# Kernel optimization log

Measured on AMD Instinct MI355X. Metric: run time of the kernel, lower is better.

The kernel has to match this reference:

```python
import jax, jax.numpy as jnp
import numpy as np

N, B, C, H = 2048, 2, 1024, 16
HD = C // H


def setup_inputs() -> dict:
    key = jax.random.key(0)
    ks = jax.random.split(key, 11)
    s = 0.02
    return {
        "query": jax.random.normal(ks[0], (N, B, C), jnp.float32),
        "key": jax.random.normal(ks[1], (N, B, C), jnp.float32),
        "value": jax.random.normal(ks[2], (B, N, C), jnp.float32),
        "num_heads": H,
        "Wq": jax.random.normal(ks[3], (C, C), jnp.float32) * s,
        "bq": jnp.zeros((C,), jnp.float32),
        "Wk": jax.random.normal(ks[4], (C, HD), jnp.float32) * s,
        "bk": jnp.zeros((HD,), jnp.float32),
        "Wv": jax.random.normal(ks[5], (C, HD), jnp.float32) * s,
        "bv": jnp.zeros((HD,), jnp.float32),
        "Wp": jax.random.normal(ks[6], (C, C), jnp.float32) * s,
        "bp": jnp.zeros((C,), jnp.float32),
    }


def reference(query, key, value, num_heads, Wq, bq, Wk, bk, Wv, bv, Wp, bp):
    # query/key arrive seq-first (N,B,C); permute to batch-first as in torch code
    k_in = jnp.transpose(key, (1, 0, 2))    # (B, Nk, C)
    q_in = jnp.transpose(query, (1, 0, 2))  # (B, Nq, C)
    Bsz, Nq, Cd = q_in.shape
    hd = Cd // num_heads
    scale = hd ** -0.5

    # shared single K/V head (MQA)
    k = k_in @ Wk + bk                      # (B, Nk, hd)
    v = value @ Wv + bv                     # (B, Nk, hd)
    q = (q_in @ Wq + bq).reshape(Bsz, Nq, num_heads, hd)
    q = jnp.transpose(q, (0, 2, 1, 3)) * scale  # (B, H, Nq, hd)

    attn = jnp.einsum('bhqd,bkd->bhqk', q, k)   # (B, H, Nq, Nk)
    attn = jax.nn.softmax(attn, axis=-1)
    x = jnp.einsum('bhqk,bkd->bhqd', attn, v)   # (B, H, Nq, hd)
    x = jnp.transpose(x, (0, 2, 1, 3)).reshape(Bsz, Nq, Cd)
    x = x @ Wp + bp
    return jnp.transpose(x, (1, 0, 2))          # (Nq, B, C)
```

## Files before the change

kernel.cpp:

```cpp
#include <hip/hip_runtime.h>
#include <hip/hip_bf16.h>

#define DI __device__ __forceinline__

typedef float f32x4 __attribute__((ext_vector_type(4)));
typedef float f32x16 __attribute__((ext_vector_type(16)));
typedef short s16x8 __attribute__((ext_vector_type(8)));
typedef unsigned short u16x4 __attribute__((ext_vector_type(4)));
typedef unsigned long long u64;


DI unsigned short f2bf(float x) {
  union { float f; unsigned u; } v; v.f = x;
  unsigned r = 0x7fffu + ((v.u >> 16) & 1u);
  return (unsigned short)((v.u + r) >> 16);
}

DI unsigned cvtpk(float lo, float hi) {
  unsigned u;
  asm("v_cvt_pk_bf16_f32 %0, %1, %2" : "=v"(u) : "v"(lo), "v"(hi));
  return u;
}

DI f32x16 zero16() {
  f32x16 z;
#pragma unroll
  for (int i = 0; i < 16; ++i) z[i] = 0.f;
  return z;
}

DI float max16(const f32x16& a) {
  float m0 = fmaxf(a[0], a[1]),  m1 = fmaxf(a[2], a[3]);
  float m2 = fmaxf(a[4], a[5]),  m3 = fmaxf(a[6], a[7]);
  float m4 = fmaxf(a[8], a[9]),  m5 = fmaxf(a[10], a[11]);
  float m6 = fmaxf(a[12], a[13]), m7 = fmaxf(a[14], a[15]);
  m0 = fmaxf(m0, m1); m2 = fmaxf(m2, m3); m4 = fmaxf(m4, m5); m6 = fmaxf(m6, m7);
  return fmaxf(fmaxf(m0, m2), fmaxf(m4, m6));
}

DI float sum16(const f32x16& a) {
  float s0 = a[0] + a[1],  s1 = a[2] + a[3];
  float s2 = a[4] + a[5],  s3 = a[6] + a[7];
  float s4 = a[8] + a[9],  s5 = a[10] + a[11];
  float s6 = a[12] + a[13], s7 = a[14] + a[15];
  s0 += s1; s2 += s3; s4 += s5; s6 += s7;
  return (s0 + s2) + (s4 + s6);
}

DI void gll16(const void* g, void* l) {
  __builtin_amdgcn_global_load_lds(
      (const __attribute__((address_space(1))) void*)g,
      (__attribute__((address_space(3))) void*)l, 16, 0, 0);
}

DI f32x16 mfma32(s16x8 a, s16x8 b, f32x16 c) {
  return __builtin_amdgcn_mfma_f32_32x32x16_bf16(a, b, c, 0, 0, 0);
}

DI f32x4 mfma16(s16x8 a, s16x8 b, f32x4 c) {
  return __builtin_amdgcn_mfma_f32_16x16x32_bf16(a, b, c, 0, 0, 0);
}

__global__ __launch_bounds__(256) void wconv_kernel(
    const float* __restrict__ Wq, const float* __restrict__ Wk,
    const float* __restrict__ Wv, const float* __restrict__ Wp,
    unsigned short* __restrict__ WqT, unsigned short* __restrict__ WkT,
    unsigned short* __restrict__ WvT, unsigned short* __restrict__ WpT)
{
  int bid = blockIdx.x;
  const float* W; unsigned short* WT; int Ncols; int base;
  if (bid < 512)       { W = Wq; WT = WqT; Ncols = 1024; base = bid; }
  else if (bid < 1024) { W = Wp; WT = WpT; Ncols = 1024; base = bid - 512; }
  else if (bid < 1056) { W = Wk; WT = WkT; Ncols = 64;   base = bid - 1024; }
  else                 { W = Wv; WT = WvT; Ncols = 64;   base = bid - 1056; }
  int nb = base >> 5, kb = base & 31;
  int n = nb * 64 + (threadIdx.x & 63);
  int k = kb * 32 + (threadIdx.x >> 6) * 8;
  float f[8];
#pragma unroll
  for (int i = 0; i < 8; ++i) f[i] = W[(size_t)(k + i) * Ncols + n];
  union { unsigned u[4]; s16x8 v; } x;
#pragma unroll
  for (int i = 0; i < 4; ++i) x.u[i] = cvtpk(f[2 * i], f[2 * i + 1]);
  *(s16x8*)(WT + (size_t)n * 1024 + k) = x.v;
}

__global__ __launch_bounds__(256) void cvt1_kernel(
    const float* __restrict__ q, unsigned short* __restrict__ qbf)
{
  int gid = blockIdx.x * 256 + threadIdx.x;
  int row = gid >> 7;
  int c8 = (gid & 127) << 3;
  int b = row >> 11, n = row & 2047;
  size_t soff = ((size_t)n * 2 + b) * 1024 + c8;
  f32x4 v0 = *(const f32x4*)(q + soff);
  f32x4 v1 = *(const f32x4*)(q + soff + 4);
  union { unsigned u[4]; s16x8 v; } x;
  x.u[0] = cvtpk(v0.x, v0.y); x.u[1] = cvtpk(v0.z, v0.w);
  x.u[2] = cvtpk(v1.x, v1.y); x.u[3] = cvtpk(v1.z, v1.w);
  *(s16x8*)(qbf + (size_t)row * 1024 + c8) = x.v;
}

template<int MODE>
__global__ __launch_bounds__(256) void gemm16_kernel(
    const unsigned short* __restrict__ A, const unsigned short* __restrict__ Bt,
    const float* __restrict__ bias, void* __restrict__ Cpv, float scale)
{
  __shared__ __align__(16) unsigned short Asub[2][128 * 64];
  __shared__ __align__(16) unsigned short Bsub[2][64 * 64];

  const int tid = threadIdx.x;
  const int lane = tid & 63, wave = tid >> 6;
  const int l16 = lane & 15, kq = lane >> 4;
  const int wr = wave >> 1, wc = wave & 1;
  const int row0 = blockIdx.x * 128;
  const int col0 = blockIdx.y * 64;

  f32x4 acc[4][2];
#pragma unroll
  for (int mi = 0; mi < 4; ++mi)
#pragma unroll
    for (int nj = 0; nj < 2; ++nj) acc[mi][nj] = f32x4{0.f, 0.f, 0.f, 0.f};

  auto STAGE = [&](int bf, int kt) {
    const int k0 = kt * 64;
#pragma unroll
    for (int i = 0; i < 4; ++i) {
      int o = i * 4096 + tid * 16;
      int r = o >> 7, c = (o & 127) >> 1;
      gll16(A + (size_t)(row0 + r) * 1024 + k0 + c,
            (char*)Asub[bf] + i * 4096 + wave * 1024);
    }
#pragma unroll
    for (int i = 0; i < 2; ++i) {
      int o = i * 4096 + tid * 16;
      int r = o >> 7, c = (o & 127) >> 1;
      gll16(Bt + (size_t)(col0 + r) * 1024 + k0 + c,
            (char*)Bsub[bf] + i * 4096 + wave * 1024);
    }
  };

  STAGE(0, 0);
  __syncthreads();
  int cur = 0;
  for (int kt = 0; kt < 16; ++kt) {
    if (kt + 1 < 16) STAGE(cur ^ 1, kt + 1);
#pragma unroll
    for (int ks = 0; ks < 2; ++ks) {
      s16x8 af[4]; s16x8 bf2[2];
#pragma unroll
      for (int mi = 0; mi < 4; ++mi)
        af[mi] = *(const s16x8*)(Asub[cur] + (wr * 64 + mi * 16 + l16) * 64 + ks * 32 + kq * 8);
#pragma unroll
      for (int nj = 0; nj < 2; ++nj)
        bf2[nj] = *(const s16x8*)(Bsub[cur] + (wc * 32 + nj * 16 + l16) * 64 + ks * 32 + kq * 8);
#pragma unroll
      for (int mi = 0; mi < 4; ++mi)
#pragma unroll
        for (int nj = 0; nj < 2; ++nj)
          acc[mi][nj] = mfma16(af[mi], bf2[nj], acc[mi][nj]);
    }
    __syncthreads();
    cur ^= 1;
  }

#pragma unroll
  for (int mi = 0; mi < 4; ++mi)
#pragma unroll
  for (int nj = 0; nj < 2; ++nj) {
    int col = col0 + wc * 32 + nj * 16 + l16;
    int rowb = row0 + wr * 64 + mi * 16 + kq * 4;
    float bv = bias[col];
#pragma unroll
    for (int r = 0; r < 4; ++r) {
      int row = rowb + r;
      float val = acc[mi][nj][r] + bv;
      if constexpr (MODE == 0) {
        ((unsigned short*)Cpv)[(size_t)row * 1024 + col] = f2bf(val * scale);
      } else {
        ((float*)Cpv)[(size_t)(row & 2047) * 2048 + (size_t)(row >> 11) * 1024 + col] = val;
      }
    }
  }
}

__global__ __launch_bounds__(256) void gemmkv_kernel(
    const float* __restrict__ Akey, const float* __restrict__ Aval,
    const unsigned short* __restrict__ Wk, const unsigned short* __restrict__ Wv,
    float* __restrict__ part)
{
  __shared__ __align__(16) unsigned short Asub[2][64 * 64];
  __shared__ __align__(16) unsigned short Bsub[2][64 * 64];

  const int tid = threadIdx.x;
  const int lane = tid & 63, wave = tid >> 6;
  const int l16 = lane & 15, kq = lane >> 4;
  const int wr = wave >> 1, wc = wave & 1;
  const int sel = blockIdx.y;
  const float* Af = sel ? Aval : Akey;
  const unsigned short* Bt = sel ? Wv : Wk;
  const int row0 = blockIdx.x * 64;
  const int kt0 = blockIdx.z * 4, kt1 = kt0 + 4;

  const int ar = tid >> 2, ac = (tid & 3) * 16;
  const int gm = row0 + ar;
  const size_t grow = sel ? (size_t)gm * 1024
                          : (size_t)((gm & 2047) * 2 + (gm >> 11)) * 1024;

  auto LOADA = [&](int kt, f32x4* a4) {
#pragma unroll
    for (int i = 0; i < 4; ++i)
      a4[i] = *(const f32x4*)(Af + grow + kt * 64 + ac + i * 4);
  };
  auto WRITEA = [&](int bf, const f32x4* a4) {
    union { unsigned u[8]; s16x8 v[2]; } x;
#pragma unroll
    for (int i = 0; i < 4; ++i) {
      x.u[2 * i]     = cvtpk(a4[i].x, a4[i].y);
      x.u[2 * i + 1] = cvtpk(a4[i].z, a4[i].w);
    }
    *(s16x8*)(Asub[bf] + ar * 64 + ac)     = x.v[0];
    *(s16x8*)(Asub[bf] + ar * 64 + ac + 8) = x.v[1];
  };
  auto STAGEB = [&](int bf, int kt) {
#pragma unroll
    for (int i = 0; i < 2; ++i) {
      int o = i * 4096 + tid * 16;
      int r = o >> 7, c = (o & 127) >> 1;
      gll16(Bt + (size_t)r * 1024 + kt * 64 + c,
            (char*)Bsub[bf] + i * 4096 + wave * 1024);
    }
  };

  f32x4 acc[2][2];
#pragma unroll
  for (int mi = 0; mi < 2; ++mi)
#pragma unroll
    for (int nj = 0; nj < 2; ++nj) acc[mi][nj] = f32x4{0.f, 0.f, 0.f, 0.f};

  f32x4 a4[4];
  LOADA(kt0, a4);
  STAGEB(0, kt0);
  WRITEA(0, a4);
  __syncthreads();
  int cur = 0;
  for (int kt = kt0; kt < kt1; ++kt) {
    if (kt + 1 < kt1) { LOADA(kt + 1, a4); STAGEB(cur ^ 1, kt + 1); }
#pragma unroll
    for (int ks = 0; ks < 2; ++ks) {
      s16x8 af[2]; s16x8 bf2[2];
#pragma unroll
      for (int mi = 0; mi < 2; ++mi)
        af[mi] = *(const s16x8*)(Asub[cur] + (wr * 32 + mi * 16 + l16) * 64 + ks * 32 + kq * 8);
#pragma unroll
      for (int nj = 0; nj < 2; ++nj)
        bf2[nj] = *(const s16x8*)(Bsub[cur] + (wc * 32 + nj * 16 + l16) * 64 + ks * 32 + kq * 8);
#pragma unroll
      for (int mi = 0; mi < 2; ++mi)
#pragma unroll
        for (int nj = 0; nj < 2; ++nj)
          acc[mi][nj] = mfma16(af[mi], bf2[nj], acc[mi][nj]);
    }
    if (kt + 1 < kt1) WRITEA(cur ^ 1, a4);
    __syncthreads();
    cur ^= 1;
  }

#pragma unroll
  for (int mi = 0; mi < 2; ++mi)
#pragma unroll
  for (int nj = 0; nj < 2; ++nj) {
    int col = wc * 32 + nj * 16 + l16;
    int rowb = row0 + wr * 32 + mi * 16 + kq * 4;
#pragma unroll
    for (int r = 0; r < 4; ++r)
      part[(((size_t)blockIdx.z * 2 + sel) * 4096 + rowb + r) * 64 + col] = acc[mi][nj][r];
  }
}

__global__ __launch_bounds__(256) void kvreduce_kernel(
    const float* __restrict__ part, const float* __restrict__ bk,
    const float* __restrict__ bv, unsigned short* __restrict__ kproj,
    unsigned short* __restrict__ vprojT)
{
  int gid = blockIdx.x * 256 + threadIdx.x;
  int kv = gid >> 18;
  int rem = gid & 262143;
  int row = rem >> 6, col = rem & 63;
  float s = 0.f;
#pragma unroll
  for (int z = 0; z < 4; ++z)
    s += part[(((size_t)z * 2 + kv) * 4096 + row) * 64 + col];
  s += (kv ? bv : bk)[col];
  if (kv == 0)
    kproj[(size_t)row * 64 + col] = f2bf(s);
  else
    vprojT[(size_t)(row >> 11) * 131072 + (size_t)col * 2048 + (row & 2047)] = f2bf(s);
}

__global__ __launch_bounds__(512, 4) void attn_kernel(
    const unsigned short* __restrict__ qp, const unsigned short* __restrict__ kp,
    const unsigned short* __restrict__ vpt, unsigned short* __restrict__ xout)
{
  constexpr int KSTR = 72;
  __shared__ unsigned short SM[36864];
#define KBUF(c, hh) (SM + ((c) * 2 + (hh)) * (64 * KSTR))
#define VBUF(c, hh) (SM + 18432 + ((c) * 2 + (hh)) * (64 * KSTR))

  const int tid = threadIdx.x;
  const int lane = tid & 63, wave = tid >> 6;
  const int lq = lane & 31, hi = lane >> 5;
  const int qsub = wave & 3, half = wave >> 2;
  const int b = blockIdx.y >> 4, h = blockIdx.y & 15;
  const int q0 = blockIdx.x * 128 + qsub * 32;
  const size_t qrow = (size_t)(b * 2048 + q0 + lq);

  s16x8 qf[4];
#pragma unroll
  for (int s = 0; s < 4; ++s)
    qf[s] = *(const s16x8*)(qp + qrow * 1024 + h * 64 + s * 16 + hi * 8);

  f32x16 xacc0 = zero16(), xacc1 = zero16();
  float mrun = -1e30f, ssum = 0.f;

  const unsigned short* kb = kp + (size_t)b * (2048 * 64);
  const unsigned short* vb = vpt + (size_t)b * (64 * 2048);

  const int srow = tid >> 3;
  const int scol = (tid & 7) * 8;

  s16x8 kA, kB, vA, vB;
  {
    kA = *(const s16x8*)(kb + (size_t)srow * 64 + scol);
    kB = *(const s16x8*)(kb + (size_t)(16 * 64 + srow) * 64 + scol);
    vA = *(const s16x8*)(vb + (size_t)srow * 2048 + scol);
    vB = *(const s16x8*)(vb + (size_t)srow * 2048 + 16 * 64 + scol);
    *(s16x8*)(KBUF(0, 0) + srow * KSTR + scol) = kA;
    *(s16x8*)(KBUF(0, 1) + srow * KSTR + scol) = kB;
    *(s16x8*)(VBUF(0, 0) + srow * KSTR + scol) = vA;
    *(s16x8*)(VBUF(0, 1) + srow * KSTR + scol) = vB;
  }
  int cur = 0;

  for (int it = 0; it < 16; ++it) {
    __syncthreads();
    if (it + 1 < 16) {
      kA = *(const s16x8*)(kb + (size_t)((it + 1) * 64 + srow) * 64 + scol);
      kB = *(const s16x8*)(kb + (size_t)((it + 17) * 64 + srow) * 64 + scol);
      vA = *(const s16x8*)(vb + (size_t)srow * 2048 + (it + 1) * 64 + scol);
      vB = *(const s16x8*)(vb + (size_t)srow * 2048 + (it + 17) * 64 + scol);
    }
    const unsigned short* Kc = KBUF(cur, half);
    const unsigned short* Vc = VBUF(cur, half);

    f32x16 sacc0 = zero16(), sacc1 = zero16();
    __builtin_amdgcn_s_setprio(1);
#pragma unroll
    for (int s = 0; s < 4; ++s) {
      int c = s * 16 + hi * 8;
      s16x8 kf0 = *(const s16x8*)(Kc + lq * KSTR + c);
      s16x8 kf1 = *(const s16x8*)(Kc + (32 + lq) * KSTR + c);
      sacc0 = mfma32(kf0, qf[s], sacc0);
      sacc1 = mfma32(kf1, qf[s], sacc1);
    }
    __builtin_amdgcn_s_setprio(0);

    float tm = fmaxf(max16(sacc0), max16(sacc1));
    tm = fmaxf(tm, __shfl_xor(tm, 32));
    if (!__all(tm <= mrun + 8.f)) {
      float mnew = fmaxf(mrun, tm);
      float alpha = __builtin_amdgcn_exp2f(mrun - mnew);
      ssum *= alpha;
#pragma unroll
      for (int e = 0; e < 16; ++e) { xacc0[e] *= alpha; xacc1[e] *= alpha; }
      mrun = mnew;
    }
    f32x16 p0, p1;
#pragma unroll
    for (int e = 0; e < 16; ++e) p0[e] = __builtin_amdgcn_exp2f(sacc0[e] - mrun);
#pragma unroll
    for (int e = 0; e < 16; ++e) p1[e] = __builtin_amdgcn_exp2f(sacc1[e] - mrun);
    float tsum = sum16(p0) + sum16(p1);
    tsum += __shfl_xor(tsum, 32);
    ssum += tsum;

    s16x8 pb[4];
#pragma unroll
    for (int grp = 0; grp < 4; ++grp) {
      const f32x16& pp = (grp < 2) ? p0 : p1;
      const int eb = (grp & 1) * 8;
      unsigned A  = cvtpk(pp[eb + 0], pp[eb + 1]);
      unsigned Bw = cvtpk(pp[eb + 2], pp[eb + 3]);
      unsigned Cw = cvtpk(pp[eb + 4], pp[eb + 5]);
      unsigned Dw = cvtpk(pp[eb + 6], pp[eb + 7]);
      unsigned rA = (unsigned)__shfl_xor((int)(hi ? A : Cw), 32);
      unsigned rB = (unsigned)__shfl_xor((int)(hi ? Bw : Dw), 32);
      union { unsigned u[4]; s16x8 v; } pk_;
      pk_.u[0] = hi ? rA : A;
      pk_.u[1] = hi ? rB : Bw;
      pk_.u[2] = hi ? Cw : rA;
      pk_.u[3] = hi ? Dw : rB;
      pb[grp] = pk_.v;
    }

    __builtin_amdgcn_s_setprio(1);
#pragma unroll
    for (int kvs = 0; kvs < 4; ++kvs) {
      int c = kvs * 16 + hi * 8;
      s16x8 vf0 = *(const s16x8*)(Vc + lq * KSTR + c);
      s16x8 vf1 = *(const s16x8*)(Vc + (32 + lq) * KSTR + c);
      xacc0 = mfma32(vf0, pb[kvs], xacc0);
      xacc1 = mfma32(vf1, pb[kvs], xacc1);
    }
    __builtin_amdgcn_s_setprio(0);

    if (it + 1 < 16) {
      *(s16x8*)(KBUF(cur ^ 1, 0) + srow * KSTR + scol) = kA;
      *(s16x8*)(KBUF(cur ^ 1, 1) + srow * KSTR + scol) = kB;
      *(s16x8*)(VBUF(cur ^ 1, 0) + srow * KSTR + scol) = vA;
      *(s16x8*)(VBUF(cur ^ 1, 1) + srow * KSTR + scol) = vB;
      cur ^= 1;
    }
  }

  __syncthreads();
  float* msc = (float*)SM;
  const int mi_ = (qsub * 64 + lane) * 37;
  if (half == 1) {
#pragma unroll
    for (int e = 0; e < 16; ++e) { msc[mi_ + e] = xacc0[e]; msc[mi_ + 16 + e] = xacc1[e]; }
    msc[mi_ + 32] = mrun;
    msc[mi_ + 33] = ssum;
  }
  __syncthreads();
  if (half == 0) {
    float pm = msc[mi_ + 32], ps = msc[mi_ + 33];
    float mf = fmaxf(mrun, pm);
    float aa = __builtin_amdgcn_exp2f(mrun - mf);
    float bb = __builtin_amdgcn_exp2f(pm - mf);
    float inv = 1.0f / (ssum * aa + ps * bb);
#pragma unroll
    for (int dj = 0; dj < 2; ++dj) {
      const f32x16 xa = dj ? xacc1 : xacc0;
#pragma unroll
      for (int g = 0; g < 4; ++g) {
        u16x4 o4;
#pragma unroll
        for (int r = 0; r < 4; ++r) {
          int e = g * 4 + r;
          float merged = xa[e] * aa + msc[mi_ + dj * 16 + e] * bb;
          o4[r] = f2bf(merged * inv);
        }
        int d0 = dj * 32 + 8 * g + 4 * hi;
        *(u16x4*)(xout + qrow * 1024 + h * 64 + d0) = o4;
      }
    }
  }
#undef KBUF
#undef VBUF
}

extern "C" void kernel_launch(void* const* d_in, const int* in_sizes, int n_in,
                              void* d_out, int out_size, void* d_ws, size_t ws_size,
                              hipStream_t stream)
{
  const float* query = (const float*)d_in[0];
  const float* key   = (const float*)d_in[1];
  const float* value = (const float*)d_in[2];
  const float* Wq = (const float*)d_in[4];
  const float* bq = (const float*)d_in[5];
  const float* Wk = (const float*)d_in[6];
  const float* bk = (const float*)d_in[7];
  const float* Wv = (const float*)d_in[8];
  const float* bv = (const float*)d_in[9];
  const float* Wp = (const float*)d_in[10];
  const float* bp = (const float*)d_in[11];

  char* ws = (char*)d_ws;
  unsigned short* WqT    = (unsigned short*)(ws);
  unsigned short* WpT    = (unsigned short*)(ws + (2u << 20));
  unsigned short* WkT    = (unsigned short*)(ws + (4u << 20));
  unsigned short* WvT    = (unsigned short*)(ws + (4u << 20) + (128u << 10));
  unsigned short* kproj  = (unsigned short*)(ws + (5u << 20));
  unsigned short* vprojT = (unsigned short*)(ws + (5u << 20) + (512u << 10));
  unsigned short* qproj  = (unsigned short*)(ws + (6u << 20));
  unsigned short* xbuf   = (unsigned short*)(ws + (15u << 20));
  float*          part   = (float*)xbuf;
  unsigned short* qbf    = (unsigned short*)d_out;

  wconv_kernel<<<dim3(1088), 256, 0, stream>>>(Wq, Wk, Wv, Wp, WqT, WkT, WvT, WpT);
  cvt1_kernel<<<dim3(2048), 256, 0, stream>>>(query, qbf);

  const float qscale = 0.18033688011112042f;
  gemm16_kernel<0><<<dim3(32, 16), 256, 0, stream>>>(qbf, WqT, bq, qproj, qscale);
  gemmkv_kernel<<<dim3(64, 2, 4), 256, 0, stream>>>(key, value, WkT, WvT, part);
  kvreduce_kernel<<<dim3(2048), 256, 0, stream>>>(part, bk, bv, kproj, vprojT);
  attn_kernel<<<dim3(16, 32), 512, 0, stream>>>(qproj, kproj, vprojT, xbuf);
  gemm16_kernel<2><<<dim3(32, 16), 256, 0, stream>>>(xbuf, WpT, bp, d_out, 1.0f);
}
```

Baseline: 121.9 us.

## Fuse query fp32-to-bf16 conversion into Q projection and merge Q/KV GEMM launches

```diff
diff --git a/kernel.cpp b/kernel.cpp
--- a/kernel.cpp
+++ b/kernel.cpp
@@ -22,6 +22,12 @@
   return u;
 }
 
+DI float max3f(float a, float b, float c) {
+  float d;
+  asm("v_max3_f32 %0, %1, %2, %3" : "=v"(d) : "v"(a), "v"(b), "v"(c));
+  return d;
+}
+
 DI f32x16 zero16() {
   f32x16 z;
 #pragma unroll
@@ -29,13 +35,15 @@
   return z;
 }
 
-DI float max16(const f32x16& a) {
-  float m0 = fmaxf(a[0], a[1]),  m1 = fmaxf(a[2], a[3]);
-  float m2 = fmaxf(a[4], a[5]),  m3 = fmaxf(a[6], a[7]);
-  float m4 = fmaxf(a[8], a[9]),  m5 = fmaxf(a[10], a[11]);
-  float m6 = fmaxf(a[12], a[13]), m7 = fmaxf(a[14], a[15]);
-  m0 = fmaxf(m0, m1); m2 = fmaxf(m2, m3); m4 = fmaxf(m4, m5); m6 = fmaxf(m6, m7);
-  return fmaxf(fmaxf(m0, m2), fmaxf(m4, m6));
+DI float max16_3(const f32x16& a) {
+  float m0 = max3f(a[0], a[1], a[2]);
+  float m1 = max3f(a[3], a[4], a[5]);
+  float m2 = max3f(a[6], a[7], a[8]);
+  float m3 = max3f(a[9], a[10], a[11]);
+  float m4 = max3f(a[12], a[13], a[14]);
+  float n0 = max3f(m0, m1, m2);
+  float n1 = max3f(m3, m4, a[15]);
+  return fmaxf(n0, n1);
 }
 
 DI float sum16(const f32x16& a) {
@@ -85,127 +93,22 @@
   *(s16x8*)(WT + (size_t)n * 1024 + k) = x.v;
 }
 
-__global__ __launch_bounds__(256) void cvt1_kernel(
-    const float* __restrict__ q, unsigned short* __restrict__ qbf)
-{
-  int gid = blockIdx.x * 256 + threadIdx.x;
-  int row = gid >> 7;
-  int c8 = (gid & 127) << 3;
-  int b = row >> 11, n = row & 2047;
-  size_t soff = ((size_t)n * 2 + b) * 1024 + c8;
-  f32x4 v0 = *(const f32x4*)(q + soff);
-  f32x4 v1 = *(const f32x4*)(q + soff + 4);
-  union { unsigned u[4]; s16x8 v; } x;
-  x.u[0] = cvtpk(v0.x, v0.y); x.u[1] = cvtpk(v0.z, v0.w);
-  x.u[2] = cvtpk(v1.x, v1.y); x.u[3] = cvtpk(v1.z, v1.w);
-  *(s16x8*)(qbf + (size_t)row * 1024 + c8) = x.v;
-}
-
 template<int MODE>
-__global__ __launch_bounds__(256) void gemm16_kernel(
-    const unsigned short* __restrict__ A, const unsigned short* __restrict__ Bt,
-    const float* __restrict__ bias, void* __restrict__ Cpv, float scale)
-{
-  __shared__ __align__(16) unsigned short Asub[2][128 * 64];
-  __shared__ __align__(16) unsigned short Bsub[2][64 * 64];
-
+DI void proj_body(const float* __restrict__ Af, const unsigned short* __restrict__ Bt,
+                  const float* __restrict__ bias, void* __restrict__ out,
+                  float scale, int bx, int cb, int kt0, int kt1, int zslot,
+                  bool remap, unsigned short* As, unsigned short* Bs)
+{
   const int tid = threadIdx.x;
   const int lane = tid & 63, wave = tid >> 6;
   const int l16 = lane & 15, kq = lane >> 4;
   const int wr = wave >> 1, wc = wave & 1;
-  const int row0 = blockIdx.x * 128;
-  const int col0 = blockIdx.y * 64;
-
-  f32x4 acc[4][2];
-#pragma unroll
-  for (int mi = 0; mi < 4; ++mi)
-#pragma unroll
-    for (int nj = 0; nj < 2; ++nj) acc[mi][nj] = f32x4{0.f, 0.f, 0.f, 0.f};
-
-  auto STAGE = [&](int bf, int kt) {
-    const int k0 = kt * 64;
-#pragma unroll
-    for (int i = 0; i < 4; ++i) {
-      int o = i * 4096 + tid * 16;
-      int r = o >> 7, c = (o & 127) >> 1;
-      gll16(A + (size_t)(row0 + r) * 1024 + k0 + c,
-            (char*)Asub[bf] + i * 4096 + wave * 1024);
-    }
-#pragma unroll
-    for (int i = 0; i < 2; ++i) {
-      int o = i * 4096 + tid * 16;
-      int r = o >> 7, c = (o & 127) >> 1;
-      gll16(Bt + (size_t)(col0 + r) * 1024 + k0 + c,
-            (char*)Bsub[bf] + i * 4096 + wave * 1024);
-    }
-  };
-
-  STAGE(0, 0);
-  __syncthreads();
-  int cur = 0;
-  for (int kt = 0; kt < 16; ++kt) {
-    if (kt + 1 < 16) STAGE(cur ^ 1, kt + 1);
-#pragma unroll
-    for (int ks = 0; ks < 2; ++ks) {
-      s16x8 af[4]; s16x8 bf2[2];
-#pragma unroll
-      for (int mi = 0; mi < 4; ++mi)
-        af[mi] = *(const s16x8*)(Asub[cur] + (wr * 64 + mi * 16 + l16) * 64 + ks * 32 + kq * 8);
-#pragma unroll
-      for (int nj = 0; nj < 2; ++nj)
-        bf2[nj] = *(const s16x8*)(Bsub[cur] + (wc * 32 + nj * 16 + l16) * 64 + ks * 32 + kq * 8);
-#pragma unroll
-      for (int mi = 0; mi < 4; ++mi)
-#pragma unroll
-        for (int nj = 0; nj < 2; ++nj)
-          acc[mi][nj] = mfma16(af[mi], bf2[nj], acc[mi][nj]);
-    }
-    __syncthreads();
-    cur ^= 1;
-  }
-
-#pragma unroll
-  for (int mi = 0; mi < 4; ++mi)
-#pragma unroll
-  for (int nj = 0; nj < 2; ++nj) {
-    int col = col0 + wc * 32 + nj * 16 + l16;
-    int rowb = row0 + wr * 64 + mi * 16 + kq * 4;
-    float bv = bias[col];
-#pragma unroll
-    for (int r = 0; r < 4; ++r) {
-      int row = rowb + r;
-      float val = acc[mi][nj][r] + bv;
-      if constexpr (MODE == 0) {
-        ((unsigned short*)Cpv)[(size_t)row * 1024 + col] = f2bf(val * scale);
-      } else {
-        ((float*)Cpv)[(size_t)(row & 2047) * 2048 + (size_t)(row >> 11) * 1024 + col] = val;
-      }
-    }
-  }
-}
-
-__global__ __launch_bounds__(256) void gemmkv_kernel(
-    const float* __restrict__ Akey, const float* __restrict__ Aval,
-    const unsigned short* __restrict__ Wk, const unsigned short* __restrict__ Wv,
-    float* __restrict__ part)
-{
-  __shared__ __align__(16) unsigned short Asub[2][64 * 64];
-  __shared__ __align__(16) unsigned short Bsub[2][64 * 64];
-
-  const int tid = threadIdx.x;
-  const int lane = tid & 63, wave = tid >> 6;
-  const int l16 = lane & 15, kq = lane >> 4;
-  const int wr = wave >> 1, wc = wave & 1;
-  const int sel = blockIdx.y;
-  const float* Af = sel ? Aval : Akey;
-  const unsigned short* Bt = sel ? Wv : Wk;
-  const int row0 = blockIdx.x * 64;
-  const int kt0 = blockIdx.z * 4, kt1 = kt0 + 4;
+  const int row0 = bx * 64;
 
   const int ar = tid >> 2, ac = (tid & 3) * 16;
   const int gm = row0 + ar;
-  const size_t grow = sel ? (size_t)gm * 1024
-                          : (size_t)((gm & 2047) * 2 + (gm >> 11)) * 1024;
+  const size_t grow = remap ? (size_t)((gm & 2047) * 2 + (gm >> 11)) * 1024
+                            : (size_t)gm * 1024;
 
   auto LOADA = [&](int kt, f32x4* a4) {
 #pragma unroll
@@ -219,8 +122,8 @@
       x.u[2 * i]     = cvtpk(a4[i].x, a4[i].y);
       x.u[2 * i + 1] = cvtpk(a4[i].z, a4[i].w);
     }
-    *(s16x8*)(Asub[bf] + ar * 64 + ac)     = x.v[0];
-    *(s16x8*)(Asub[bf] + ar * 64 + ac + 8) = x.v[1];
+    *(s16x8*)(As + bf * 4096 + ar * 64 + ac)     = x.v[0];
+    *(s16x8*)(As + bf * 4096 + ar * 64 + ac + 8) = x.v[1];
   };
   auto STAGEB = [&](int bf, int kt) {
 #pragma unroll
@@ -228,7 +131,7 @@
       int o = i * 4096 + tid * 16;
       int r = o >> 7, c = (o & 127) >> 1;
       gll16(Bt + (size_t)r * 1024 + kt * 64 + c,
-            (char*)Bsub[bf] + i * 4096 + wave * 1024);
+            (char*)Bs + bf * 8192 + i * 4096 + wave * 1024);
     }
   };
 
@@ -251,10 +154,10 @@
       s16x8 af[2]; s16x8 bf2[2];
 #pragma unroll
       for (int mi = 0; mi < 2; ++mi)
-        af[mi] = *(const s16x8*)(Asub[cur] + (wr * 32 + mi * 16 + l16) * 64 + ks * 32 + kq * 8);
+        af[mi] = *(const s16x8*)(As + cur * 4096 + (wr * 32 + mi * 16 + l16) * 64 + ks * 32 + kq * 8);
 #pragma unroll
       for (int nj = 0; nj < 2; ++nj)
-        bf2[nj] = *(const s16x8*)(Bsub[cur] + (wc * 32 + nj * 16 + l16) * 64 + ks * 32 + kq * 8);
+        bf2[nj] = *(const s16x8*)(Bs + cur * 4096 + (wc * 32 + nj * 16 + l16) * 64 + ks * 32 + kq * 8);
 #pragma unroll
       for (int mi = 0; mi < 2; ++mi)
 #pragma unroll
@@ -273,8 +176,113 @@
     int col = wc * 32 + nj * 16 + l16;
     int rowb = row0 + wr * 32 + mi * 16 + kq * 4;
 #pragma unroll
-    for (int r = 0; r < 4; ++r)
-      part[(((size_t)blockIdx.z * 2 + sel) * 4096 + rowb + r) * 64 + col] = acc[mi][nj][r];
+    for (int r = 0; r < 4; ++r) {
+      if constexpr (MODE == 0) {
+        float val = (acc[mi][nj][r] + bias[cb + col]) * scale;
+        ((unsigned short*)out)[(size_t)(rowb + r) * 1024 + cb + col] = f2bf(val);
+      } else {
+        ((float*)out)[(((size_t)zslot) * 4096 + rowb + r) * 64 + col] = acc[mi][nj][r];
+      }
+    }
+  }
+}
+
+__global__ __launch_bounds__(256) void gemmproj_kernel(
+    const float* __restrict__ query, const unsigned short* __restrict__ WqT,
+    const float* __restrict__ bq, unsigned short* __restrict__ qproj, float qscale,
+    const float* __restrict__ key, const float* __restrict__ value,
+    const unsigned short* __restrict__ WkT, const unsigned short* __restrict__ WvT,
+    float* __restrict__ part)
+{
+  __shared__ __align__(16) unsigned short SMEM[16384];
+  int bid = blockIdx.x;
+  if (bid < 1024) {
+    int bx = bid & 63, by = bid >> 6;
+    proj_body<0>(query, WqT + (size_t)by * 64 * 1024, bq, qproj, qscale,
+                 bx, by * 64, 0, 16, 0, true, SMEM, SMEM + 8192);
+  } else {
+    int idx = bid - 1024;
+    int bx = idx & 63, sel = (idx >> 6) & 1, bz = idx >> 7;
+    proj_body<1>(sel ? value : key, sel ? WvT : WkT, nullptr, part,
+                 1.0f, bx, 0, bz * 4, bz * 4 + 4, bz * 2 + sel, sel == 0,
+                 SMEM, SMEM + 8192);
+  }
+}
+
+__global__ __launch_bounds__(256) void gemmout_kernel(
+    const unsigned short* __restrict__ A, const unsigned short* __restrict__ Bt,
+    const float* __restrict__ bias, float* __restrict__ Cpv)
+{
+  __shared__ __align__(16) unsigned short As[2][128 * 64];
+  __shared__ __align__(16) unsigned short Bs[2][64 * 64];
+
+  const int tid = threadIdx.x;
+  const int lane = tid & 63, wave = tid >> 6;
+  const int l16 = lane & 15, kq = lane >> 4;
+  const int wr = wave >> 1, wc = wave & 1;
+  const int row0 = blockIdx.x * 128;
+  const int col0 = blockIdx.y * 64;
+
+  f32x4 acc[4][2];
+#pragma unroll
+  for (int mi = 0; mi < 4; ++mi)
+#pragma unroll
+    for (int nj = 0; nj < 2; ++nj) acc[mi][nj] = f32x4{0.f, 0.f, 0.f, 0.f};
+
+  auto STAGE = [&](int bf, int kt) {
+    const int k0 = kt * 64;
+#pragma unroll
+    for (int i = 0; i < 4; ++i) {
+      int o = i * 4096 + tid * 16;
+      int r = o >> 7, c = (o & 127) >> 1;
+      gll16(A + (size_t)(row0 + r) * 1024 + k0 + c,
+            (char*)As[bf] + i * 4096 + wave * 1024);
+    }
+#pragma unroll
+    for (int i = 0; i < 2; ++i) {
+      int o = i * 4096 + tid * 16;
+      int r = o >> 7, c = (o & 127) >> 1;
+      gll16(Bt + (size_t)(col0 + r) * 1024 + k0 + c,
+            (char*)Bs[bf] + i * 4096 + wave * 1024);
+    }
+  };
+
+  STAGE(0, 0);
+  __syncthreads();
+  int cur = 0;
+  for (int kt = 0; kt < 16; ++kt) {
+    if (kt + 1 < 16) STAGE(cur ^ 1, kt + 1);
+#pragma unroll
+    for (int ks = 0; ks < 2; ++ks) {
+      s16x8 af[4]; s16x8 bf2[2];
+#pragma unroll
+      for (int mi = 0; mi < 4; ++mi)
+        af[mi] = *(const s16x8*)(As[cur] + (wr * 64 + mi * 16 + l16) * 64 + ks * 32 + kq * 8);
+#pragma unroll
+      for (int nj = 0; nj < 2; ++nj)
+        bf2[nj] = *(const s16x8*)(Bs[cur] + (wc * 32 + nj * 16 + l16) * 64 + ks * 32 + kq * 8);
+#pragma unroll
+      for (int mi = 0; mi < 4; ++mi)
+#pragma unroll
+        for (int nj = 0; nj < 2; ++nj)
+          acc[mi][nj] = mfma16(af[mi], bf2[nj], acc[mi][nj]);
+    }
+    __syncthreads();
+    cur ^= 1;
+  }
+
+#pragma unroll
+  for (int mi = 0; mi < 4; ++mi)
+#pragma unroll
+  for (int nj = 0; nj < 2; ++nj) {
+    int col = col0 + wc * 32 + nj * 16 + l16;
+    int rowb = row0 + wr * 64 + mi * 16 + kq * 4;
+    float bv = bias[col];
+#pragma unroll
+    for (int r = 0; r < 4; ++r) {
+      int row = rowb + r;
+      Cpv[(size_t)(row & 2047) * 2048 + (size_t)(row >> 11) * 1024 + col] = acc[mi][nj][r] + bv;
+    }
   }
 }
 
@@ -365,7 +373,7 @@
     }
     __builtin_amdgcn_s_setprio(0);
 
-    float tm = fmaxf(max16(sacc0), max16(sacc1));
+    float tm = fmaxf(max16_3(sacc0), max16_3(sacc1));
     tm = fmaxf(tm, __shfl_xor(tm, 32));
     if (!__all(tm <= mrun + 8.f)) {
       float mnew = fmaxf(mrun, tm);
@@ -486,15 +494,13 @@
   unsigned short* qproj  = (unsigned short*)(ws + (6u << 20));
   unsigned short* xbuf   = (unsigned short*)(ws + (15u << 20));
   float*          part   = (float*)xbuf;
-  unsigned short* qbf    = (unsigned short*)d_out;
 
   wconv_kernel<<<dim3(1088), 256, 0, stream>>>(Wq, Wk, Wv, Wp, WqT, WkT, WvT, WpT);
-  cvt1_kernel<<<dim3(2048), 256, 0, stream>>>(query, qbf);
 
   const float qscale = 0.18033688011112042f;
-  gemm16_kernel<0><<<dim3(32, 16), 256, 0, stream>>>(qbf, WqT, bq, qproj, qscale);
-  gemmkv_kernel<<<dim3(64, 2, 4), 256, 0, stream>>>(key, value, WkT, WvT, part);
+  gemmproj_kernel<<<dim3(1536), 256, 0, stream>>>(
+      query, WqT, bq, qproj, qscale, key, value, WkT, WvT, part);
   kvreduce_kernel<<<dim3(2048), 256, 0, stream>>>(part, bk, bv, kproj, vprojT);
   attn_kernel<<<dim3(16, 32), 512, 0, stream>>>(qproj, kproj, vprojT, xbuf);
-  gemm16_kernel<2><<<dim3(32, 16), 256, 0, stream>>>(xbuf, WpT, bp, d_out, 1.0f);
-}
+  gemmout_kernel<<<dim3(32, 16), 256, 0, stream>>>(xbuf, WpT, bp, (float*)d_out);
+}
```

Result: no change. 119.6 us (-1.9%).
